# Performance work log

Measured on AMD Instinct MI355X. Metric: run time of the kernel, lower is better.

## Reference

```python
import jax, jax.numpy as jnp
import numpy as np

B, S, HID = 2, 2048, 2048
NH, NKV, DH = 32, 8, 64
WIN = 1024


def rotate_half(x):
    x1, x2 = x[..., : x.shape[-1] // 2], x[..., x.shape[-1] // 2:]
    return jnp.concatenate((-x2, x1), axis=-1)


def setup_inputs() -> dict:
    key = jax.random.key(0)
    ks = jax.random.split(key, 8)
    hidden_states = jax.random.normal(ks[0], (B, S, HID), dtype=jnp.float32)
    # real RoPE tables: [B, S, DH]
    inv_freq = 1.0 / (10000.0 ** (np.arange(0, DH, 2, dtype=np.float32) / DH))
    ang = np.arange(S, dtype=np.float32)[:, None] * inv_freq[None, :]  # [S, DH/2]
    emb = np.concatenate([ang, ang], axis=-1)  # [S, DH]
    cos = jnp.broadcast_to(jnp.asarray(np.cos(emb)), (B, S, DH))
    sin = jnp.broadcast_to(jnp.asarray(np.sin(emb)), (B, S, DH))
    sc = 0.02
    Wq = jax.random.normal(ks[1], (NH * DH, HID), dtype=jnp.float32) * sc
    Wk = jax.random.normal(ks[2], (NKV * DH, HID), dtype=jnp.float32) * sc
    Wv = jax.random.normal(ks[3], (NKV * DH, HID), dtype=jnp.float32) * sc
    Wo = jax.random.normal(ks[4], (HID, NH * DH), dtype=jnp.float32) * sc
    return {"hidden_states": hidden_states, "cos": cos, "sin": sin,
            "Wq": Wq, "Wk": Wk, "Wv": Wv, "Wo": Wo}


def sliding_window_mask(q_len, k_len, dtype):
    half = WIN // 2
    qi = jnp.arange(q_len)[:, None]
    ki = jnp.arange(k_len)[None, :]
    last = jnp.clip(qi + half, None, k_len - 1)
    first = jnp.clip(qi - half, 0, None)
    visible = (ki >= first) & (ki <= last)
    minv = jnp.finfo(dtype).min
    return jnp.where(visible, jnp.array(0.0, dtype), jnp.array(minv, dtype))  # [q_len, k_len]


def reference(hidden_states, cos, sin, Wq, Wk, Wv, Wo):
    b, s, _ = hidden_states.shape
    scale = DH ** -0.5
    q = (hidden_states @ Wq.T).reshape(b, s, NH, DH).transpose(0, 2, 1, 3)   # [B,NH,S,DH]
    k = (hidden_states @ Wk.T).reshape(b, s, NKV, DH).transpose(0, 2, 1, 3)  # [B,NKV,S,DH]
    v = (hidden_states @ Wv.T).reshape(b, s, NKV, DH).transpose(0, 2, 1, 3)
    c, sn = cos[:, None, :, :], sin[:, None, :, :]  # broadcast over heads
    q = q * c + rotate_half(q) * sn
    k = k * c + rotate_half(k) * sn
    groups = NH // NKV
    k = jnp.repeat(k, groups, axis=1)  # [B,NH,S,DH]
    v = jnp.repeat(v, groups, axis=1)
    mask = sliding_window_mask(s, s, hidden_states.dtype)  # [S,S]
    scores = jnp.einsum("bhqd,bhkd->bhqk", q, k) * scale + mask  # dense quadratic bias add
    attn = jax.nn.softmax(scores, axis=-1)
    out = jnp.einsum("bhqk,bhkd->bhqd", attn, v)
    out = out.transpose(0, 2, 1, 3).reshape(b, s, NH * DH)
    return out @ Wo.T
```

## Files before the change

kernel.cpp:

```cpp
#include <hip/hip_runtime.h>
#include <hip/hip_bf16.h>
#include <stdint.h>
#include <stddef.h>

#define S_LEN 2048
#define HIDDEN 2048
#define NHEAD 32
#define NKVH 8
#define DHEAD 64
#define BATCH 2
#define HALFW 512
#define QSCALE 0.18033688011112042f

typedef __attribute__((ext_vector_type(4))) float f32x4;
typedef __attribute__((ext_vector_type(8))) short short8;
typedef __attribute__((ext_vector_type(4))) short short4v;
typedef __attribute__((ext_vector_type(2))) unsigned int u32x2;

__device__ __forceinline__ unsigned short f2bf(float f) {
  unsigned u = __builtin_bit_cast(unsigned, f);
  u += 0x7fffu + ((u >> 16) & 1u);
  return (unsigned short)(u >> 16);
}
__device__ __forceinline__ float bf2f(unsigned short h) {
  unsigned u = ((unsigned)h) << 16;
  return __builtin_bit_cast(float, u);
}
__device__ __forceinline__ unsigned cvt_pk_bf16(float lo, float hi) {
  unsigned r;
  asm("v_cvt_pk_bf16_f32 %0, %1, %2" : "=v"(r) : "v"(lo), "v"(hi));
  return r;
}

__global__ void k_cvt5(const float* __restrict__ s0, const float* __restrict__ s1,
                       const float* __restrict__ s2, const float* __restrict__ s3,
                       const float* __restrict__ s4,
                       unsigned short* __restrict__ d0, unsigned short* __restrict__ d1,
                       unsigned short* __restrict__ d2, unsigned short* __restrict__ d3,
                       unsigned short* __restrict__ d4) {
  int i = blockIdx.x * blockDim.x + threadIdx.x;
#pragma unroll 1
  for (int it = 0; it < 9; ++it, i += 524288) {
    const float* src;
    unsigned short* dst;
    int base;
    if (i < 2097152)      { src = s0; dst = d0; base = 0; }
    else if (i < 3145728) { src = s1; dst = d1; base = 2097152; }
    else if (i < 3407872) { src = s2; dst = d2; base = 3145728; }
    else if (i < 3670016) { src = s3; dst = d3; base = 3407872; }
    else                  { src = s4; dst = d4; base = 3670016; }
    int j = i - base;
    float4 v = reinterpret_cast<const float4*>(src)[j];
    short4v o;
    o[0] = (short)f2bf(v.x);
    o[1] = (short)f2bf(v.y);
    o[2] = (short)f2bf(v.z);
    o[3] = (short)f2bf(v.w);
    reinterpret_cast<short4v*>(dst)[j] = o;
  }
}

template <int CSTORE_F32>
__global__ __launch_bounds__(256) void k_gemm_bt(const unsigned short* __restrict__ A,
                                                 const unsigned short* __restrict__ Bw,
                                                 void* __restrict__ Cout,
                                                 int M, int N, int K) {
  __shared__ unsigned short As[128][32];
  __shared__ unsigned short Bs[128][32];
  const int tid = threadIdx.x;
  const int wid = tid >> 6;
  const int lane = tid & 63;
  const int l15 = lane & 15;
  const int lhi = lane >> 4;
  const int bm = blockIdx.y * 128;
  const int bn = blockIdx.x * 128;
  const int wm = (wid >> 1) * 64;
  const int wn = (wid & 1) * 64;
  f32x4 acc[4][4] = {};

  for (int k0 = 0; k0 < K; k0 += 32) {
#pragma unroll
    for (int i = 0; i < 2; ++i) {
      int u = i * 256 + tid;
      int row = u >> 2, c8 = u & 3;
      const unsigned short* ga = A + (size_t)(bm + row) * K + k0 + c8 * 8;
      const unsigned short* gb = Bw + (size_t)(bn + row) * K + k0 + c8 * 8;
      __builtin_amdgcn_global_load_lds(
          (const __attribute__((address_space(1))) unsigned int*)(const void*)ga,
          (__attribute__((address_space(3))) unsigned int*)(void*)((char*)&As[0][0] + i * 4096 + wid * 1024),
          16, 0, 0);
      __builtin_amdgcn_global_load_lds(
          (const __attribute__((address_space(1))) unsigned int*)(const void*)gb,
          (__attribute__((address_space(3))) unsigned int*)(void*)((char*)&Bs[0][0] + i * 4096 + wid * 1024),
          16, 0, 0);
    }
    __syncthreads();

    short8 af[4], bfr[4];
#pragma unroll
    for (int m = 0; m < 4; ++m)
      af[m] = *reinterpret_cast<const short8*>(&As[wm + m * 16 + l15][lhi * 8]);
#pragma unroll
    for (int n = 0; n < 4; ++n)
      bfr[n] = *reinterpret_cast<const short8*>(&Bs[wn + n * 16 + l15][lhi * 8]);
#pragma unroll
    for (int m = 0; m < 4; ++m)
#pragma unroll
      for (int n = 0; n < 4; ++n)
        acc[m][n] = __builtin_amdgcn_mfma_f32_16x16x32_bf16(af[m], bfr[n], acc[m][n], 0, 0, 0);
    __syncthreads();
  }

#pragma unroll
  for (int m = 0; m < 4; ++m) {
#pragma unroll
    for (int r = 0; r < 4; ++r) {
      int row = bm + wm + m * 16 + lhi * 4 + r;
#pragma unroll
      for (int n = 0; n < 4; ++n) {
        int col = bn + wn + n * 16 + l15;
        float v = acc[m][n][r];
        if (CSTORE_F32)
          ((float*)Cout)[(size_t)row * N + col] = v;
        else
          ((unsigned short*)Cout)[(size_t)row * N + col] = f2bf(v);
      }
    }
  }
}

__global__ void k_rope(const unsigned short* __restrict__ qkv,
                       const float* __restrict__ cosb, const float* __restrict__ sinb,
                       unsigned short* __restrict__ Qr, unsigned short* __restrict__ Kr) {
  int idx = blockIdx.x * blockDim.x + threadIdx.x;
  if (idx >= BATCH * S_LEN * 40 * 32) return;
  int d = idx & 31;
  int hh = (idx >> 5) % 40;
  int bs = idx / (40 * 32);
  int s = bs % S_LEN, b = bs / S_LEN;
  int row = b * S_LEN + s;
  float c = cosb[row * DHEAD + d];
  float sn = sinb[row * DHEAD + d];
  int col = (hh < 32) ? (hh * DHEAD + d) : (2048 + (hh - 32) * DHEAD + d);
  const unsigned short* p = qkv + (size_t)row * 3072;
  float x1 = bf2f(p[col]);
  float x2 = bf2f(p[col + 32]);
  float o1 = x1 * c - x2 * sn;
  float o2 = x2 * c + x1 * sn;
  if (hh < 32) {
    size_t o = ((size_t)(b * NHEAD + hh) * S_LEN + s) * DHEAD + d;
    Qr[o] = f2bf(o1 * QSCALE);
    Qr[o + 32] = f2bf(o2 * QSCALE);
  } else {
    size_t o = ((size_t)(b * NKVH + (hh - 32)) * S_LEN + s) * DHEAD + d;
    Kr[o] = f2bf(o1);
    Kr[o + 32] = f2bf(o2);
  }
}

__global__ void k_vt(const unsigned short* __restrict__ qkv, unsigned short* __restrict__ Vt) {
  __shared__ unsigned short t[64][68];
  int s0 = blockIdx.x * 64;
  int b = blockIdx.y >> 3, hk = blockIdx.y & 7;
  int tid = threadIdx.x;
#pragma unroll
  for (int it = 0; it < 4; ++it) {
    int u = it * 256 + tid;
    int srow = u >> 4, c4 = u & 15;
    short4v v = *reinterpret_cast<const short4v*>(
        &qkv[(size_t)(b * S_LEN + s0 + srow) * 3072 + 2560 + hk * 64 + c4 * 4]);
    *reinterpret_cast<short4v*>(&t[srow][c4 * 4]) = v;
  }
  __syncthreads();
#pragma unroll
  for (int it = 0; it < 4; ++it) {
    int u = it * 256 + tid;
    int d = u >> 4, s4 = u & 15;
    short4v v;
#pragma unroll
    for (int j = 0; j < 4; ++j) v[j] = t[s4 * 4 + j][d];
    *reinterpret_cast<short4v*>(
        &Vt[((size_t)(b * NKVH + hk) * DHEAD + d) * S_LEN + s0 + s4 * 4]) = v;
  }
}

__global__ __launch_bounds__(256, 4) void k_attn(const unsigned short* __restrict__ Qr,
                                                 const unsigned short* __restrict__ Kr,
                                                 const unsigned short* __restrict__ Vt,
                                                 unsigned short* __restrict__ AO) {
  __shared__ unsigned short Ks[2][64][64];
  __shared__ unsigned short Vs[2][64][64];
  __shared__ unsigned short Pl[4][16][64];

  const int tid = threadIdx.x, w = tid >> 6, lane = tid & 63;
  const int l15 = lane & 15, lhi = lane >> 4;

  int p = blockIdx.x;
  int L = (p & 7) * 256 + (p >> 3);
  int g = L >> 7;
  int b = g >> 3, hk = g & 7;
  int r_ = L & 127;
  int h = hk * 4 + (r_ >> 5);
  int q0b = (r_ & 31) * 64;
  const int qw = q0b + w * 16;

  const unsigned short* Qh = Qr + (size_t)(b * NHEAD + h) * S_LEN * DHEAD;
  const unsigned short* Kh = Kr + (size_t)(b * NKVH + hk) * S_LEN * DHEAD;
  const unsigned short* Vh = Vt + (size_t)(b * NKVH + hk) * DHEAD * S_LEN;

  short8 qf[2];
#pragma unroll
  for (int c = 0; c < 2; ++c)
    qf[c] = *reinterpret_cast<const short8*>(&Qh[(size_t)(qw + l15) * DHEAD + c * 32 + lhi * 8]);

  f32x4 o[4] = {};
  float den = 0.f;
  const int q = qw + l15;
  const int kvisLo = q - HALFW, kvisHi = q + HALFW;

  char* plbase = (char*)&Pl[w][0][0];
  const int swz = (l15 & 7) << 4;

  int klo = q0b - HALFW; if (klo < 0) klo = 0;
  klo &= ~63;
  int khi = q0b + 63 + HALFW; if (khi > S_LEN - 1) khi = S_LEN - 1;
  const int nt = ((khi + 1 - klo) + 63) >> 6;

  auto stage = [&](int bufidx, int kbb) {
#pragma unroll
    for (int i = 0; i < 2; ++i) {
      int u = i * 256 + tid;
      int row = u >> 3, c16 = u & 7;
      int sc = c16 ^ (row & 7);
      __builtin_amdgcn_global_load_lds(
          (const __attribute__((address_space(1))) unsigned int*)(const void*)
              (Kh + (size_t)(kbb + row) * DHEAD + sc * 8),
          (__attribute__((address_space(3))) unsigned int*)(void*)
              ((char*)&Ks[bufidx][0][0] + u * 16),
          16, 0, 0);
      __builtin_amdgcn_global_load_lds(
          (const __attribute__((address_space(1))) unsigned int*)(const void*)
              (Vh + (size_t)row * S_LEN + kbb + sc * 8),
          (__attribute__((address_space(3))) unsigned int*)(void*)
              ((char*)&Vs[bufidx][0][0] + u * 16),
          16, 0, 0);
    }
  };

  int cur = 0;
  stage(0, klo);
  __syncthreads();

  for (int t = 0; t < nt; ++t) {
    const int kb = klo + t * 64;
    if (t + 1 < nt) stage(cur ^ 1, kb + 64);

    f32x4 sacc[4] = {};
#pragma unroll
    for (int hh = 0; hh < 4; ++hh) {
      int kr = hh * 16 + l15;
      const char* kbase = (const char*)&Ks[cur][0][0] + kr * 128;
      short8 kf0 = *reinterpret_cast<const short8*>(kbase + ((lhi ^ (kr & 7)) * 16));
      short8 kf1 = *reinterpret_cast<const short8*>(kbase + (((4 + lhi) ^ (kr & 7)) * 16));
      sacc[hh] = __builtin_amdgcn_mfma_f32_16x16x32_bf16(kf0, qf[0], sacc[hh], 0, 0, 0);
      sacc[hh] = __builtin_amdgcn_mfma_f32_16x16x32_bf16(kf1, qf[1], sacc[hh], 0, 0, 0);
    }

    const bool inter = (kb >= qw + 15 - HALFW) && (kb + 63 <= qw + HALFW);
    if (inter) {
#pragma unroll
      for (int hh = 0; hh < 4; ++hh) {
        float p0 = __builtin_amdgcn_exp2f(sacc[hh][0]);
        float p1 = __builtin_amdgcn_exp2f(sacc[hh][1]);
        float p2 = __builtin_amdgcn_exp2f(sacc[hh][2]);
        float p3 = __builtin_amdgcn_exp2f(sacc[hh][3]);
        den += (p0 + p1) + (p2 + p3);
        u32x2 pw;
        pw[0] = cvt_pk_bf16(p0, p1);
        pw[1] = cvt_pk_bf16(p2, p3);
        *(u32x2*)(plbase + ((l15 * 128 + hh * 32 + lhi * 8) ^ swz)) = pw;
      }
    } else {
#pragma unroll
      for (int hh = 0; hh < 4; ++hh) {
        float pp[4];
#pragma unroll
        for (int r = 0; r < 4; ++r) {
          int key = kb + hh * 16 + lhi * 4 + r;
          bool vis = (key >= kvisLo) && (key <= kvisHi);
          pp[r] = vis ? __builtin_amdgcn_exp2f(sacc[hh][r]) : 0.0f;
        }
        den += (pp[0] + pp[1]) + (pp[2] + pp[3]);
        u32x2 pw;
        pw[0] = cvt_pk_bf16(pp[0], pp[1]);
        pw[1] = cvt_pk_bf16(pp[2], pp[3]);
        *(u32x2*)(plbase + ((l15 * 128 + hh * 32 + lhi * 8) ^ swz)) = pw;
      }
    }
    asm volatile("s_waitcnt lgkmcnt(0)" ::: "memory");
    __builtin_amdgcn_sched_barrier(0);

    short8 pf0 = *reinterpret_cast<const short8*>(plbase + ((l15 * 128 + lhi * 16) ^ swz));
    short8 pf1 = *reinterpret_cast<const short8*>(plbase + ((l15 * 128 + 64 + lhi * 16) ^ swz));
#pragma unroll
    for (int c = 0; c < 4; ++c) {
      int d = c * 16 + l15;
      const char* vbase = (const char*)&Vs[cur][0][0] + d * 128;
      short8 vf0 = *reinterpret_cast<const short8*>(vbase + ((lhi ^ (d & 7)) * 16));
      short8 vf1 = *reinterpret_cast<const short8*>(vbase + (((4 + lhi) ^ (d & 7)) * 16));
      o[c] = __builtin_amdgcn_mfma_f32_16x16x32_bf16(pf0, vf0, o[c], 0, 0, 0);
      o[c] = __builtin_amdgcn_mfma_f32_16x16x32_bf16(pf1, vf1, o[c], 0, 0, 0);
    }

    __syncthreads();
    cur ^= 1;
  }

  den += __shfl_xor(den, 16);
  den += __shfl_xor(den, 32);

#pragma unroll
  for (int r = 0; r < 4; ++r) {
    int qo = qw + lhi * 4 + r;
    float dr = __shfl(den, lhi * 4 + r, 64);
    float dinv = 1.0f / dr;
#pragma unroll
    for (int c = 0; c < 4; ++c)
      AO[(size_t)(b * S_LEN + qo) * HIDDEN + h * DHEAD + c * 16 + l15] = f2bf(o[c][r] * dinv);
  }
}

extern "C" void kernel_launch(void* const* d_in, const int* in_sizes, int n_in,
                              void* d_out, int out_size, void* d_ws, size_t ws_size,
                              hipStream_t stream) {
  const float* hs   = (const float*)d_in[0];
  const float* cosb = (const float*)d_in[1];
  const float* sinb = (const float*)d_in[2];
  const float* Wq   = (const float*)d_in[3];
  const float* Wk   = (const float*)d_in[4];
  const float* Wv   = (const float*)d_in[5];
  const float* Wo   = (const float*)d_in[6];

  char* ws = (char*)d_ws;
  unsigned short* Xbf  = (unsigned short*)(ws);
  unsigned short* Wqkv = (unsigned short*)(ws + 16777216);
  unsigned short* QKV  = (unsigned short*)(ws + 16777216 + 12582912);
  unsigned short* Wob  = (unsigned short*)(ws + 16777216 + 12582912 + 25165824);

  unsigned short* Qr = Xbf;
  unsigned short* Kr = Wqkv;
  unsigned short* Vt = (unsigned short*)(ws + 16777216 + 4194304);
  unsigned short* AO = QKV;

  k_cvt5<<<2048, 256, 0, stream>>>(hs, Wq, Wk, Wv, Wo,
                                   Xbf, Wqkv, Wqkv + 4194304, Wqkv + 5242880, Wob);

  k_gemm_bt<0><<<dim3(3072 / 128, 4096 / 128), 256, 0, stream>>>(Xbf, Wqkv, (void*)QKV, 4096, 3072, 2048);

  k_rope<<<(BATCH * S_LEN * 40 * 32) / 256, 256, 0, stream>>>(QKV, cosb, sinb, Qr, Kr);
  k_vt<<<dim3(S_LEN / 64, BATCH * NKVH), 256, 0, stream>>>(QKV, Vt);

  k_attn<<<BATCH * NHEAD * (S_LEN / 64), 256, 0, stream>>>(Qr, Kr, Vt, AO);

  k_gemm_bt<1><<<dim3(2048 / 128, 4096 / 128), 256, 0, stream>>>(AO, Wob, d_out, 4096, 2048, 2048);
}
```

Measured before the change: 216.7 us.

## Replace GEMM with 256x256-tile, 4-stage pipelined 8-wave kernel; add MFMA priority hints

```diff
diff --git a/kernel.cpp b/kernel.cpp
--- a/kernel.cpp
+++ b/kernel.cpp
@@ -61,65 +61,105 @@
 }
 
 template <int CSTORE_F32>
-__global__ __launch_bounds__(256) void k_gemm_bt(const unsigned short* __restrict__ A,
-                                                 const unsigned short* __restrict__ Bw,
-                                                 void* __restrict__ Cout,
-                                                 int M, int N, int K) {
-  __shared__ unsigned short As[128][32];
-  __shared__ unsigned short Bs[128][32];
+__global__ __launch_bounds__(512, 2) void k_gemm8(const unsigned short* __restrict__ A,
+                                                  const unsigned short* __restrict__ Bw,
+                                                  void* __restrict__ Cout,
+                                                  int M, int N, int K, int ntx) {
+  __shared__ unsigned short As[4][8192];
+  __shared__ unsigned short Bs[4][8192];
   const int tid = threadIdx.x;
-  const int wid = tid >> 6;
-  const int lane = tid & 63;
-  const int l15 = lane & 15;
-  const int lhi = lane >> 4;
-  const int bm = blockIdx.y * 128;
-  const int bn = blockIdx.x * 128;
-  const int wm = (wid >> 1) * 64;
-  const int wn = (wid & 1) * 64;
-  f32x4 acc[4][4] = {};
-
-  for (int k0 = 0; k0 < K; k0 += 32) {
+  const int w = tid >> 6, lane = tid & 63;
+  const int l15 = lane & 15, lhi = lane >> 4;
+  const int wm = w >> 2, wn = w & 3;
+
+  const int cpx = (int)gridDim.x >> 3;
+  const int bid = blockIdx.x;
+  const int swz = (bid & 7) * cpx + (bid >> 3);
+  const int ty = swz / ntx, tx = swz - ty * ntx;
+  const int bm = ty * 256, bn = tx * 256;
+
+  const int NH = K >> 5;
+
+  const int abase = (l15 & 7) * 16 + lhi * 128 + (l15 >> 3) * 512 + wm * 8192;
+  const int bbase = (l15 & 7) * 16 + lhi * 128 + (l15 >> 3) * 512 + wn * 4096;
+
+  f32x4 acc[8][4] = {};
+
+  auto stage = [&](int hs) {
+    const int kb = hs << 5;
+    const int sl = hs & 3;
 #pragma unroll
     for (int i = 0; i < 2; ++i) {
-      int u = i * 256 + tid;
-      int row = u >> 2, c8 = u & 3;
-      const unsigned short* ga = A + (size_t)(bm + row) * K + k0 + c8 * 8;
-      const unsigned short* gb = Bw + (size_t)(bn + row) * K + k0 + c8 * 8;
+      int u = i * 512 + tid;
+      int row = (u & 7) | ((u >> 5) << 3);
+      int c16 = (u >> 3) & 3;
       __builtin_amdgcn_global_load_lds(
-          (const __attribute__((address_space(1))) unsigned int*)(const void*)ga,
-          (__attribute__((address_space(3))) unsigned int*)(void*)((char*)&As[0][0] + i * 4096 + wid * 1024),
+          (const __attribute__((address_space(1))) unsigned int*)(const void*)
+              (A + (size_t)(bm + row) * K + kb + c16 * 8),
+          (__attribute__((address_space(3))) unsigned int*)(void*)
+              ((char*)&As[sl][0] + u * 16),
           16, 0, 0);
       __builtin_amdgcn_global_load_lds(
-          (const __attribute__((address_space(1))) unsigned int*)(const void*)gb,
-          (__attribute__((address_space(3))) unsigned int*)(void*)((char*)&Bs[0][0] + i * 4096 + wid * 1024),
+          (const __attribute__((address_space(1))) unsigned int*)(const void*)
+              (Bw + (size_t)(bn + row) * K + kb + c16 * 8),
+          (__attribute__((address_space(3))) unsigned int*)(void*)
+              ((char*)&Bs[sl][0] + u * 16),
           16, 0, 0);
     }
-    __syncthreads();
-
-    short8 af[4], bfr[4];
-#pragma unroll
-    for (int m = 0; m < 4; ++m)
-      af[m] = *reinterpret_cast<const short8*>(&As[wm + m * 16 + l15][lhi * 8]);
-#pragma unroll
-    for (int n = 0; n < 4; ++n)
-      bfr[n] = *reinterpret_cast<const short8*>(&Bs[wn + n * 16 + l15][lhi * 8]);
-#pragma unroll
-    for (int m = 0; m < 4; ++m)
-#pragma unroll
-      for (int n = 0; n < 4; ++n)
-        acc[m][n] = __builtin_amdgcn_mfma_f32_16x16x32_bf16(af[m], bfr[n], acc[m][n], 0, 0, 0);
-    __syncthreads();
-  }
-
-#pragma unroll
-  for (int m = 0; m < 4; ++m) {
+  };
+
+  auto compute = [&](int hh) {
+    const int sl = hh & 3;
+    const char* ap = (const char*)&As[sl][0] + abase;
+    const char* bp = (const char*)&Bs[sl][0] + bbase;
+    short8 av[8], bv[4];
+#pragma unroll
+    for (int mf = 0; mf < 8; ++mf) av[mf] = *(const short8*)(ap + mf * 1024);
+#pragma unroll
+    for (int nf = 0; nf < 4; ++nf) bv[nf] = *(const short8*)(bp + nf * 1024);
+    __builtin_amdgcn_s_setprio(1);
+#pragma unroll
+    for (int mf = 0; mf < 8; ++mf)
+#pragma unroll
+      for (int nf = 0; nf < 4; ++nf)
+        acc[mf][nf] = __builtin_amdgcn_mfma_f32_16x16x32_bf16(av[mf], bv[nf], acc[mf][nf], 0, 0, 0);
+    __builtin_amdgcn_s_setprio(0);
+    __builtin_amdgcn_sched_barrier(0);
+    __builtin_amdgcn_s_barrier();
+    __builtin_amdgcn_sched_barrier(0);
+  };
+
+  stage(0); stage(1); stage(2);
+
+  for (int h = 0; h < NH - 3; ++h) {
+    stage(h + 3);
+    asm volatile("s_waitcnt vmcnt(12)" ::: "memory");
+    __builtin_amdgcn_s_barrier();
+    __builtin_amdgcn_sched_barrier(0);
+    compute(h);
+  }
+  asm volatile("s_waitcnt vmcnt(8)" ::: "memory");
+  __builtin_amdgcn_s_barrier();
+  __builtin_amdgcn_sched_barrier(0);
+  compute(NH - 3);
+  asm volatile("s_waitcnt vmcnt(4)" ::: "memory");
+  __builtin_amdgcn_s_barrier();
+  __builtin_amdgcn_sched_barrier(0);
+  compute(NH - 2);
+  asm volatile("s_waitcnt vmcnt(0)" ::: "memory");
+  __builtin_amdgcn_s_barrier();
+  __builtin_amdgcn_sched_barrier(0);
+  compute(NH - 1);
+
+#pragma unroll
+  for (int mf = 0; mf < 8; ++mf) {
 #pragma unroll
     for (int r = 0; r < 4; ++r) {
-      int row = bm + wm + m * 16 + lhi * 4 + r;
-#pragma unroll
-      for (int n = 0; n < 4; ++n) {
-        int col = bn + wn + n * 16 + l15;
-        float v = acc[m][n][r];
+      int row = bm + wm * 128 + mf * 16 + lhi * 4 + r;
+#pragma unroll
+      for (int nf = 0; nf < 4; ++nf) {
+        int col = bn + wn * 64 + nf * 16 + l15;
+        float v = acc[mf][nf][r];
         if (CSTORE_F32)
           ((float*)Cout)[(size_t)row * N + col] = v;
         else
@@ -219,7 +259,7 @@
   const int kvisLo = q - HALFW, kvisHi = q + HALFW;
 
   char* plbase = (char*)&Pl[w][0][0];
-  const int swz = (l15 & 7) << 4;
+  const int swzp = (l15 & 7) << 4;
 
   int klo = q0b - HALFW; if (klo < 0) klo = 0;
   klo &= ~63;
@@ -256,6 +296,7 @@
     if (t + 1 < nt) stage(cur ^ 1, kb + 64);
 
     f32x4 sacc[4] = {};
+    __builtin_amdgcn_s_setprio(1);
 #pragma unroll
     for (int hh = 0; hh < 4; ++hh) {
       int kr = hh * 16 + l15;
@@ -265,6 +306,7 @@
       sacc[hh] = __builtin_amdgcn_mfma_f32_16x16x32_bf16(kf0, qf[0], sacc[hh], 0, 0, 0);
       sacc[hh] = __builtin_amdgcn_mfma_f32_16x16x32_bf16(kf1, qf[1], sacc[hh], 0, 0, 0);
     }
+    __builtin_amdgcn_s_setprio(0);
 
     const bool inter = (kb >= qw + 15 - HALFW) && (kb + 63 <= qw + HALFW);
     if (inter) {
@@ -278,7 +320,7 @@
         u32x2 pw;
         pw[0] = cvt_pk_bf16(p0, p1);
         pw[1] = cvt_pk_bf16(p2, p3);
-        *(u32x2*)(plbase + ((l15 * 128 + hh * 32 + lhi * 8) ^ swz)) = pw;
+        *(u32x2*)(plbase + ((l15 * 128 + hh * 32 + lhi * 8) ^ swzp)) = pw;
       }
     } else {
 #pragma unroll
@@ -294,14 +336,15 @@
         u32x2 pw;
         pw[0] = cvt_pk_bf16(pp[0], pp[1]);
         pw[1] = cvt_pk_bf16(pp[2], pp[3]);
-        *(u32x2*)(plbase + ((l15 * 128 + hh * 32 + lhi * 8) ^ swz)) = pw;
+        *(u32x2*)(plbase + ((l15 * 128 + hh * 32 + lhi * 8) ^ swzp)) = pw;
       }
     }
     asm volatile("s_waitcnt lgkmcnt(0)" ::: "memory");
     __builtin_amdgcn_sched_barrier(0);
 
-    short8 pf0 = *reinterpret_cast<const short8*>(plbase + ((l15 * 128 + lhi * 16) ^ swz));
-    short8 pf1 = *reinterpret_cast<const short8*>(plbase + ((l15 * 128 + 64 + lhi * 16) ^ swz));
+    short8 pf0 = *reinterpret_cast<const short8*>(plbase + ((l15 * 128 + lhi * 16) ^ swzp));
+    short8 pf1 = *reinterpret_cast<const short8*>(plbase + ((l15 * 128 + 64 + lhi * 16) ^ swzp));
+    __builtin_amdgcn_s_setprio(1);
 #pragma unroll
     for (int c = 0; c < 4; ++c) {
       int d = c * 16 + l15;
@@ -311,6 +354,7 @@
       o[c] = __builtin_amdgcn_mfma_f32_16x16x32_bf16(pf0, vf0, o[c], 0, 0, 0);
       o[c] = __builtin_amdgcn_mfma_f32_16x16x32_bf16(pf1, vf1, o[c], 0, 0, 0);
     }
+    __builtin_amdgcn_s_setprio(0);
 
     __syncthreads();
     cur ^= 1;
@@ -355,12 +399,12 @@
   k_cvt5<<<2048, 256, 0, stream>>>(hs, Wq, Wk, Wv, Wo,
                                    Xbf, Wqkv, Wqkv + 4194304, Wqkv + 5242880, Wob);
 
-  k_gemm_bt<0><<<dim3(3072 / 128, 4096 / 128), 256, 0, stream>>>(Xbf, Wqkv, (void*)QKV, 4096, 3072, 2048);
+  k_gemm8<0><<<dim3(192), 512, 0, stream>>>(Xbf, Wqkv, (void*)QKV, 4096, 3072, 2048, 12);
 
   k_rope<<<(BATCH * S_LEN * 40 * 32) / 256, 256, 0, stream>>>(QKV, cosb, sinb, Qr, Kr);
   k_vt<<<dim3(S_LEN / 64, BATCH * NKVH), 256, 0, stream>>>(QKV, Vt);
 
   k_attn<<<BATCH * NHEAD * (S_LEN / 64), 256, 0, stream>>>(Qr, Kr, Vt, AO);
 
-  k_gemm_bt<1><<<dim3(2048 / 128, 4096 / 128), 256, 0, stream>>>(AO, Wob, d_out, 4096, 2048, 2048);
-}
+  k_gemm8<1><<<dim3(128), 512, 0, stream>>>(AO, Wob, d_out, 4096, 2048, 2048, 8);
+}
```

Result: slower. 283.0 us (+30.6%).

## Fuse RoPE and Q/K/V scatter into QKV GEMM epilogue, add MFMA priority hints

Applied to the files above, without the earlier changes.

```diff
diff --git a/kernel.cpp b/kernel.cpp
--- a/kernel.cpp
+++ b/kernel.cpp
@@ -60,10 +60,15 @@
   }
 }
 
-template <int CSTORE_F32>
+template <int MODE>
 __global__ __launch_bounds__(256) void k_gemm_bt(const unsigned short* __restrict__ A,
                                                  const unsigned short* __restrict__ Bw,
                                                  void* __restrict__ Cout,
+                                                 const float* __restrict__ cosb,
+                                                 const float* __restrict__ sinb,
+                                                 unsigned short* __restrict__ Qr,
+                                                 unsigned short* __restrict__ Kr,
+                                                 unsigned short* __restrict__ Vrow,
                                                  int M, int N, int K) {
   __shared__ unsigned short As[128][32];
   __shared__ unsigned short Bs[128][32];
@@ -111,64 +116,71 @@
     __syncthreads();
   }
 
-#pragma unroll
-  for (int m = 0; m < 4; ++m) {
-#pragma unroll
-    for (int r = 0; r < 4; ++r) {
-      int row = bm + wm + m * 16 + lhi * 4 + r;
-#pragma unroll
-      for (int n = 0; n < 4; ++n) {
-        int col = bn + wn + n * 16 + l15;
-        float v = acc[m][n][r];
-        if (CSTORE_F32)
-          ((float*)Cout)[(size_t)row * N + col] = v;
-        else
-          ((unsigned short*)Cout)[(size_t)row * N + col] = f2bf(v);
+  if (MODE == 1) {
+#pragma unroll
+    for (int m = 0; m < 4; ++m) {
+#pragma unroll
+      for (int r = 0; r < 4; ++r) {
+        int row = bm + wm + m * 16 + lhi * 4 + r;
+#pragma unroll
+        for (int n = 0; n < 4; ++n) {
+          int col = bn + wn + n * 16 + l15;
+          ((float*)Cout)[(size_t)row * N + col] = acc[m][n][r];
+        }
       }
     }
-  }
-}
-
-__global__ void k_rope(const unsigned short* __restrict__ qkv,
-                       const float* __restrict__ cosb, const float* __restrict__ sinb,
-                       unsigned short* __restrict__ Qr, unsigned short* __restrict__ Kr) {
-  int idx = blockIdx.x * blockDim.x + threadIdx.x;
-  if (idx >= BATCH * S_LEN * 40 * 32) return;
-  int d = idx & 31;
-  int hh = (idx >> 5) % 40;
-  int bs = idx / (40 * 32);
-  int s = bs % S_LEN, b = bs / S_LEN;
-  int row = b * S_LEN + s;
-  float c = cosb[row * DHEAD + d];
-  float sn = sinb[row * DHEAD + d];
-  int col = (hh < 32) ? (hh * DHEAD + d) : (2048 + (hh - 32) * DHEAD + d);
-  const unsigned short* p = qkv + (size_t)row * 3072;
-  float x1 = bf2f(p[col]);
-  float x2 = bf2f(p[col + 32]);
-  float o1 = x1 * c - x2 * sn;
-  float o2 = x2 * c + x1 * sn;
-  if (hh < 32) {
-    size_t o = ((size_t)(b * NHEAD + hh) * S_LEN + s) * DHEAD + d;
-    Qr[o] = f2bf(o1 * QSCALE);
-    Qr[o + 32] = f2bf(o2 * QSCALE);
   } else {
-    size_t o = ((size_t)(b * NKVH + (hh - 32)) * S_LEN + s) * DHEAD + d;
-    Kr[o] = f2bf(o1);
-    Kr[o + 32] = f2bf(o2);
-  }
-}
-
-__global__ void k_vt(const unsigned short* __restrict__ qkv, unsigned short* __restrict__ Vt) {
+    const int hc = (bn + wn) >> 6;
+#pragma unroll
+    for (int m = 0; m < 4; ++m) {
+#pragma unroll
+      for (int r = 0; r < 4; ++r) {
+        int row = bm + wm + m * 16 + lhi * 4 + r;
+        int b = row >> 11, s = row & 2047;
+        if (hc < 40) {
+#pragma unroll
+          for (int n = 0; n < 2; ++n) {
+            int d = n * 16 + l15;
+            float c = cosb[(size_t)row * DHEAD + d];
+            float sn = sinb[(size_t)row * DHEAD + d];
+            float x1 = acc[m][n][r];
+            float x2 = acc[m][n + 2][r];
+            float o1 = x1 * c - x2 * sn;
+            float o2 = x2 * c + x1 * sn;
+            if (hc < 32) {
+              size_t o = ((size_t)(b * NHEAD + hc) * S_LEN + s) * DHEAD + d;
+              Qr[o] = f2bf(o1 * QSCALE);
+              Qr[o + 32] = f2bf(o2 * QSCALE);
+            } else {
+              size_t o = ((size_t)(b * NKVH + (hc - 32)) * S_LEN + s) * DHEAD + d;
+              Kr[o] = f2bf(o1);
+              Kr[o + 32] = f2bf(o2);
+            }
+          }
+        } else {
+#pragma unroll
+          for (int n = 0; n < 4; ++n) {
+            int d = n * 16 + l15;
+            size_t o = ((size_t)(b * NKVH + (hc - 40)) * S_LEN + s) * DHEAD + d;
+            Vrow[o] = f2bf(acc[m][n][r]);
+          }
+        }
+      }
+    }
+  }
+}
+
+__global__ void k_vt(const unsigned short* __restrict__ Vrow, unsigned short* __restrict__ Vt) {
   __shared__ unsigned short t[64][68];
   int s0 = blockIdx.x * 64;
-  int b = blockIdx.y >> 3, hk = blockIdx.y & 7;
+  int g = blockIdx.y;
   int tid = threadIdx.x;
 #pragma unroll
   for (int it = 0; it < 4; ++it) {
     int u = it * 256 + tid;
     int srow = u >> 4, c4 = u & 15;
     short4v v = *reinterpret_cast<const short4v*>(
-        &qkv[(size_t)(b * S_LEN + s0 + srow) * 3072 + 2560 + hk * 64 + c4 * 4]);
+        &Vrow[((size_t)g * S_LEN + s0 + srow) * DHEAD + c4 * 4]);
     *reinterpret_cast<short4v*>(&t[srow][c4 * 4]) = v;
   }
   __syncthreads();
@@ -180,7 +192,7 @@
 #pragma unroll
     for (int j = 0; j < 4; ++j) v[j] = t[s4 * 4 + j][d];
     *reinterpret_cast<short4v*>(
-        &Vt[((size_t)(b * NKVH + hk) * DHEAD + d) * S_LEN + s0 + s4 * 4]) = v;
+        &Vt[((size_t)g * DHEAD + d) * S_LEN + s0 + s4 * 4]) = v;
   }
 }
 
@@ -219,7 +231,7 @@
   const int kvisLo = q - HALFW, kvisHi = q + HALFW;
 
   char* plbase = (char*)&Pl[w][0][0];
-  const int swz = (l15 & 7) << 4;
+  const int swzp = (l15 & 7) << 4;
 
   int klo = q0b - HALFW; if (klo < 0) klo = 0;
   klo &= ~63;
@@ -256,6 +268,7 @@
     if (t + 1 < nt) stage(cur ^ 1, kb + 64);
 
     f32x4 sacc[4] = {};
+    __builtin_amdgcn_s_setprio(1);
 #pragma unroll
     for (int hh = 0; hh < 4; ++hh) {
       int kr = hh * 16 + l15;
@@ -265,6 +278,7 @@
       sacc[hh] = __builtin_amdgcn_mfma_f32_16x16x32_bf16(kf0, qf[0], sacc[hh], 0, 0, 0);
       sacc[hh] = __builtin_amdgcn_mfma_f32_16x16x32_bf16(kf1, qf[1], sacc[hh], 0, 0, 0);
     }
+    __builtin_amdgcn_s_setprio(0);
 
     const bool inter = (kb >= qw + 15 - HALFW) && (kb + 63 <= qw + HALFW);
     if (inter) {
@@ -278,7 +292,7 @@
         u32x2 pw;
         pw[0] = cvt_pk_bf16(p0, p1);
         pw[1] = cvt_pk_bf16(p2, p3);
-        *(u32x2*)(plbase + ((l15 * 128 + hh * 32 + lhi * 8) ^ swz)) = pw;
+        *(u32x2*)(plbase + ((l15 * 128 + hh * 32 + lhi * 8) ^ swzp)) = pw;
       }
     } else {
 #pragma unroll
@@ -294,14 +308,15 @@
         u32x2 pw;
         pw[0] = cvt_pk_bf16(pp[0], pp[1]);
         pw[1] = cvt_pk_bf16(pp[2], pp[3]);
-        *(u32x2*)(plbase + ((l15 * 128 + hh * 32 + lhi * 8) ^ swz)) = pw;
+        *(u32x2*)(plbase + ((l15 * 128 + hh * 32 + lhi * 8) ^ swzp)) = pw;
       }
     }
     asm volatile("s_waitcnt lgkmcnt(0)" ::: "memory");
     __builtin_amdgcn_sched_barrier(0);
 
-    short8 pf0 = *reinterpret_cast<const short8*>(plbase + ((l15 * 128 + lhi * 16) ^ swz));
-    short8 pf1 = *reinterpret_cast<const short8*>(plbase + ((l15 * 128 + 64 + lhi * 16) ^ swz));
+    short8 pf0 = *reinterpret_cast<const short8*>(plbase + ((l15 * 128 + lhi * 16) ^ swzp));
+    short8 pf1 = *reinterpret_cast<const short8*>(plbase + ((l15 * 128 + 64 + lhi * 16) ^ swzp));
+    __builtin_amdgcn_s_setprio(1);
 #pragma unroll
     for (int c = 0; c < 4; ++c) {
       int d = c * 16 + l15;
@@ -311,6 +326,7 @@
       o[c] = __builtin_amdgcn_mfma_f32_16x16x32_bf16(pf0, vf0, o[c], 0, 0, 0);
       o[c] = __builtin_amdgcn_mfma_f32_16x16x32_bf16(pf1, vf1, o[c], 0, 0, 0);
     }
+    __builtin_amdgcn_s_setprio(0);
 
     __syncthreads();
     cur ^= 1;
@@ -344,23 +360,24 @@
   char* ws = (char*)d_ws;
   unsigned short* Xbf  = (unsigned short*)(ws);
   unsigned short* Wqkv = (unsigned short*)(ws + 16777216);
-  unsigned short* QKV  = (unsigned short*)(ws + 16777216 + 12582912);
-  unsigned short* Wob  = (unsigned short*)(ws + 16777216 + 12582912 + 25165824);
-
-  unsigned short* Qr = Xbf;
-  unsigned short* Kr = Wqkv;
-  unsigned short* Vt = (unsigned short*)(ws + 16777216 + 4194304);
-  unsigned short* AO = QKV;
+  unsigned short* Vt   = (unsigned short*)(ws + 29360128);
+  unsigned short* AO   = (unsigned short*)(ws + 33554432);
+  unsigned short* Wob  = (unsigned short*)(ws + 54525952);
+
+  unsigned short* Qr   = (unsigned short*)d_out;
+  unsigned short* Kr   = Qr + (size_t)BATCH * NKVH * S_LEN * DHEAD * 4;
+  unsigned short* Vrow = Kr + (size_t)BATCH * NKVH * S_LEN * DHEAD;
 
   k_cvt5<<<2048, 256, 0, stream>>>(hs, Wq, Wk, Wv, Wo,
                                    Xbf, Wqkv, Wqkv + 4194304, Wqkv + 5242880, Wob);
 
-  k_gemm_bt<0><<<dim3(3072 / 128, 4096 / 128), 256, 0, stream>>>(Xbf, Wqkv, (void*)QKV, 4096, 3072, 2048);
-
-  k_rope<<<(BATCH * S_LEN * 40 * 32) / 256, 256, 0, stream>>>(QKV, cosb, sinb, Qr, Kr);
-  k_vt<<<dim3(S_LEN / 64, BATCH * NKVH), 256, 0, stream>>>(QKV, Vt);
+  k_gemm_bt<2><<<dim3(3072 / 128, 4096 / 128), 256, 0, stream>>>(
+      Xbf, Wqkv, nullptr, cosb, sinb, Qr, Kr, Vrow, 4096, 3072, 2048);
+
+  k_vt<<<dim3(S_LEN / 64, BATCH * NKVH), 256, 0, stream>>>(Vrow, Vt);
 
   k_attn<<<BATCH * NHEAD * (S_LEN / 64), 256, 0, stream>>>(Qr, Kr, Vt, AO);
 
-  k_gemm_bt<1><<<dim3(2048 / 128, 4096 / 128), 256, 0, stream>>>(AO, Wob, d_out, 4096, 2048, 2048);
-}
+  k_gemm_bt<1><<<dim3(2048 / 128, 4096 / 128), 256, 0, stream>>>(
+      AO, Wob, d_out, nullptr, nullptr, nullptr, nullptr, nullptr, 4096, 2048, 2048);
+}
```

Measured after the change: 215.3 us. Within noise of the previous version (-0.7%).
